# Kernel tuning notes

Hardware: AMD Instinct MI355X
Metric: run time of the kernel (lower is better)

The kernel has to match this reference:

```python
import jax, jax.numpy as jnp
import numpy as np

N, E = 100000, 1600000
IN, ED, H, HL, OUT = 32, 8, 16, 64, 4
BN_EPS = 1e-5


def setup_inputs() -> dict:
    key = jax.random.key(0)
    keys = iter(jax.random.split(key, 64))

    def rn(*s):
        return jax.random.normal(next(keys), s, jnp.float32) * 0.1

    inp = {}
    inp["x"] = jax.random.normal(next(keys), (N, IN), jnp.float32)
    inp["edge_index"] = jax.random.randint(next(keys), (2, E), 0, N)
    inp["edge_attr"] = jax.random.normal(next(keys), (E, ED), jnp.float32)
    for c, din in ((1, IN), (2, H), (3, H)):
        inp[f"ew{c}"] = rn(ED, din)   # GINEConv edge lin: edge_dim -> in_channels
        inp[f"eb{c}"] = rn(din)
        inp[f"wa{c}"] = rn(din, H)    # nn Linear 1
        inp[f"ba{c}"] = rn(H)
        inp[f"g{c}"] = jnp.ones((H,), jnp.float32)    # BN gamma
        inp[f"be{c}"] = jnp.zeros((H,), jnp.float32)  # BN beta
        inp[f"m{c}"] = rn(H)                           # BN running mean
        inp[f"v{c}"] = jax.random.uniform(next(keys), (H,), jnp.float32, 0.5, 1.5)  # BN running var
        inp[f"wb{c}"] = rn(H, H)      # nn Linear 2
        inp[f"bb{c}"] = rn(H)
    inp["lw1"] = rn(3 * H, HL)
    inp["lb1"] = rn(HL)
    inp["lw2"] = rn(HL, OUT)
    inp["lb2"] = rn(OUT)
    return inp


def gine_conv(x, edge_attr, src, dst, ew, eb, wa, ba, g, be, m, v, wb, bb):
    # message: relu(x_j + lin_edge(edge_attr)); aggregate: sum at dst; eps = 0
    e = edge_attr @ ew + eb                      # [E, din]
    msg = jax.nn.relu(x[src] + e)                # [E, din]
    agg = jax.ops.segment_sum(msg, dst, num_segments=x.shape[0])  # [N, din]
    h = (x + agg) @ wa + ba                      # Linear 1
    h = (h - m) * jax.lax.rsqrt(v + BN_EPS) * g + be  # BatchNorm1d (eval)
    h = jax.nn.relu(h)
    h = jax.nn.relu(h @ wb + bb)                 # Linear 2 + ReLU
    return h


def reference(x, edge_index, edge_attr,
              ew1, eb1, wa1, ba1, g1, be1, m1, v1, wb1, bb1,
              ew2, eb2, wa2, ba2, g2, be2, m2, v2, wb2, bb2,
              ew3, eb3, wa3, ba3, g3, be3, m3, v3, wb3, bb3,
              lw1, lb1, lw2, lb2):
    src, dst = edge_index[0], edge_index[1]
    h1 = gine_conv(x, edge_attr, src, dst, ew1, eb1, wa1, ba1, g1, be1, m1, v1, wb1, bb1)
    h2 = gine_conv(h1, edge_attr, src, dst, ew2, eb2, wa2, ba2, g2, be2, m2, v2, wb2, bb2)
    h3 = gine_conv(h2, edge_attr, src, dst, ew3, eb3, wa3, ba3, g3, be3, m3, v3, wb3, bb3)
    h = jnp.concatenate((h1, h2, h3), axis=1)    # [N, 3H]
    h = jax.nn.relu(h @ lw1 + lb1)               # dropout p=0.5 is identity in eval
    return h @ lw2 + lb2                         # [N, OUT]
```

## Files before the change

### kernel.cpp

```cpp
#include <hip/hip_runtime.h>
#include <hip/hip_bf16.h>

#define BN_EPS 1e-5f
#define BINSHIFT 6
#define BINW 64
#define NBLK 256


__global__ __launch_bounds__(256)
void hist2d_kernel(const int* __restrict__ dst, int* __restrict__ histmat,
                   int E, int nbins, int chunk) {
    __shared__ int h[2048];
    for (int i = threadIdx.x; i < nbins; i += 256) h[i] = 0;
    __syncthreads();
    int b = blockIdx.x;
    int e0 = b * chunk;
    int e1 = min(E, e0 + chunk);
    for (int e = e0 + threadIdx.x; e < e1; e += 256)
        atomicAdd(&h[dst[e] >> BINSHIFT], 1);
    __syncthreads();
    int* row = histmat + (size_t)b * nbins;
    for (int i = threadIdx.x; i < nbins; i += 256) row[i] = h[i];
}

__global__ __launch_bounds__(256)
void colsum_kernel(const int* __restrict__ histmat, int* __restrict__ bincnt,
                   int nbins) {
    int bin = blockIdx.x * 256 + threadIdx.x;
    if (bin >= nbins) return;
    int s = 0;
    for (int r = 0; r < NBLK; ++r) s += histmat[(size_t)r * nbins + bin];
    bincnt[bin] = s;
}

__global__ __launch_bounds__(1024)
void bin_scan_kernel(const int* __restrict__ bincnt, int* __restrict__ binstart,
                     int nbins, int E) {
    __shared__ int a[2048];
    __shared__ int b[1024];
    int t = threadIdx.x;
    a[t]        = (t < nbins) ? bincnt[t] : 0;
    a[t + 1024] = (t + 1024 < nbins) ? bincnt[t + 1024] : 0;
    __syncthreads();
    b[t] = a[2 * t] + a[2 * t + 1];
    __syncthreads();
    for (int off = 1; off < 1024; off <<= 1) {
        int v = (t >= off) ? b[t - off] : 0;
        __syncthreads();
        b[t] += v;
        __syncthreads();
    }
    int base = (t == 0) ? 0 : b[t - 1];
    if (2 * t < nbins)     binstart[2 * t]     = base;
    if (2 * t + 1 < nbins) binstart[2 * t + 1] = base + a[2 * t];
    if (t == 0) binstart[nbins] = E;
}

__global__ __launch_bounds__(256)
void rowscan_kernel(int* __restrict__ histmat, const int* __restrict__ binstart,
                    int nbins) {
    __shared__ int a[NBLK];
    int b = blockIdx.x;
    int t = threadIdx.x;
    int v = histmat[(size_t)t * nbins + b];
    a[t] = v;
    __syncthreads();
    for (int off = 1; off < NBLK; off <<= 1) {
        int add = (t >= off) ? a[t - off] : 0;
        __syncthreads();
        a[t] += add;
        __syncthreads();
    }
    histmat[(size_t)t * nbins + b] = binstart[b] + a[t] - v;
}

__global__ __launch_bounds__(256)
void place_kernel(const int* __restrict__ src, const int* __restrict__ dst,
                  const float* __restrict__ edge_attr,
                  const int* __restrict__ histmat,
                  int* __restrict__ tmp_meta, float* __restrict__ tmp_ea,
                  int E, int nbins, int chunk) {
    __shared__ int cur[2048];
    int b = blockIdx.x;
    const int* row = histmat + (size_t)b * nbins;
    for (int i = threadIdx.x; i < nbins; i += 256) cur[i] = row[i];
    __syncthreads();
    int e0 = b * chunk;
    int e1 = min(E, e0 + chunk);
    for (int e = e0 + threadIdx.x; e < e1; e += 256) {
        int d = dst[e];
        int bin = d >> BINSHIFT;
        int pos = atomicAdd(&cur[bin], 1);
        tmp_meta[pos] = ((d & (BINW - 1)) << 20) | src[e];
        const float4* sp = (const float4*)(edge_attr + (size_t)e * 8);
        float4 a0 = sp[0], a1 = sp[1];
        float4* dp = (float4*)(tmp_ea + (size_t)pos * 8);
        dp[0] = a0;
        dp[1] = a1;
    }
}

__global__ __launch_bounds__(256)
void pass2_kernel(const int* __restrict__ binstart, const int* __restrict__ tmp_meta,
                  const float* __restrict__ tmp_ea,
                  int* __restrict__ rowstart, int* __restrict__ src_sorted,
                  float* __restrict__ ea_sorted, int N, int E) {
    __shared__ int s_cur[BINW];
    int b = blockIdx.x;
    int node0 = b << BINSHIFT;
    int e0 = binstart[b], e1 = binstart[b + 1];
    int t = threadIdx.x;

    if (t < BINW) s_cur[t] = 0;
    __syncthreads();

    for (int e = e0 + t; e < e1; e += 256)
        atomicAdd(&s_cur[tmp_meta[e] >> 20], 1);
    __syncthreads();

    if (t < BINW) {
        int val = s_cur[t];
        int inc = val;
#pragma unroll
        for (int off = 1; off < 64; off <<= 1) {
            int n = __shfl_up(inc, off);
            if (t >= off) inc += n;
        }
        int excl = e0 + inc - val;
        s_cur[t] = excl;
        int node = node0 + t;
        if (node <= N) rowstart[node] = excl;
    }
    __syncthreads();

    for (int e = e0 + t; e < e1; e += 256) {
        int mx = tmp_meta[e];
        int dl   = mx >> 20;
        int srcv = mx & 0xFFFFF;
        int fpos = atomicAdd(&s_cur[dl], 1);
        src_sorted[fpos] = srcv;
        const float4* sp = (const float4*)(tmp_ea + (size_t)e * 8);
        float4 a0 = sp[0], a1 = sp[1];
        float4* dp = (float4*)(ea_sorted + (size_t)fpos * 8);
        dp[0] = a0;
        dp[1] = a1;
    }
}

template<int DIN, int C, int S>
__global__ __launch_bounds__(256)
void gine_layer_wave(const float* __restrict__ xin,
                     const int*   __restrict__ rowstart,
                     const int*   __restrict__ src_sorted,
                     const float* __restrict__ ea_sorted,
                     const float* __restrict__ ew, const float* __restrict__ eb,
                     const float* __restrict__ wa, const float* __restrict__ ba,
                     const float* __restrict__ g, const float* __restrict__ be,
                     const float* __restrict__ m, const float* __restrict__ v,
                     const float* __restrict__ wb, const float* __restrict__ bb,
                     float* __restrict__ hout,
                     int N) {
    static_assert(C * S == 64 && C * 4 == DIN, "lane layout");
    constexpr int PAD = DIN + 1;

    __shared__ float s_wa[DIN * 16];
    __shared__ float s_wb[256];
    __shared__ float s_ba[16], s_scale[16], s_shift[16], s_bb[16];
    __shared__ float s_s[16 * PAD];
    __shared__ float s_h[16 * 17];

    int t = threadIdx.x;
    for (int idx = t; idx < DIN * 16; idx += 256) s_wa[idx] = wa[idx];
    s_wb[t] = wb[t];
    if (t < 16) {
        s_ba[t] = ba[t];
        float sc = g[t] * rsqrtf(v[t] + BN_EPS);
        s_scale[t] = sc;
        s_shift[t] = be[t] - m[t] * sc;
        s_bb[t] = bb[t];
    }

    int w    = t >> 6;
    int lane = t & 63;
    int c    = lane / S;
    int s    = lane % S;
    int c0   = c * 4;

    float ew_r[8][4];
#pragma unroll
    for (int k = 0; k < 8; ++k) {
        float4 wv = *(const float4*)(ew + k * DIN + c0);
        ew_r[k][0] = wv.x; ew_r[k][1] = wv.y; ew_r[k][2] = wv.z; ew_r[k][3] = wv.w;
    }
    float4 ebv = *(const float4*)(eb + c0);
    float eb_r[4] = {ebv.x, ebv.y, ebv.z, ebv.w};

    int node0 = blockIdx.x * 16;

#pragma unroll
    for (int q = 0; q < 4; ++q) {
        int nl = w * 4 + q;
        int i  = node0 + nl;
        float acc[4] = {0.f, 0.f, 0.f, 0.f};
        if (i < N) {
            int e0 = rowstart[i];
            int e1 = rowstart[i + 1];
            int e  = e0 + s;
            int sv = (e < e1) ? src_sorted[e] : 0;
            for (; e < e1; e += S) {
                int en = e + S;
                int sv_next = (en < e1) ? src_sorted[en] : 0;
                const float4* ep = (const float4*)(ea_sorted + (size_t)e * 8);
                float4 a0 = ep[0], a1 = ep[1];
                float4 xv = *(const float4*)(xin + (size_t)sv * DIN + c0);
                float av[8] = {a0.x, a0.y, a0.z, a0.w, a1.x, a1.y, a1.z, a1.w};
                float xr[4] = {xv.x, xv.y, xv.z, xv.w};
#pragma unroll
                for (int j = 0; j < 4; ++j) {
                    float lin = eb_r[j];
#pragma unroll
                    for (int k = 0; k < 8; ++k) lin = fmaf(av[k], ew_r[k][j], lin);
                    lin += xr[j];
                    acc[j] += (lin > 0.f ? lin : 0.f);
                }
                sv = sv_next;
            }
        }
#pragma unroll
        for (int mask = S >> 1; mask >= 1; mask >>= 1) {
#pragma unroll
            for (int j = 0; j < 4; ++j) acc[j] += __shfl_xor(acc[j], mask);
        }
        if (s == 0 && i < N) {
            float4 xi = *(const float4*)(xin + (size_t)i * DIN + c0);
            s_s[nl * PAD + c0 + 0] = acc[0] + xi.x;
            s_s[nl * PAD + c0 + 1] = acc[1] + xi.y;
            s_s[nl * PAD + c0 + 2] = acc[2] + xi.z;
            s_s[nl * PAD + c0 + 3] = acc[3] + xi.w;
        }
    }
    __syncthreads();

    int nl2 = t >> 4;
    int j   = t & 15;
    float a = s_ba[j];
#pragma unroll
    for (int k = 0; k < DIN; ++k)
        a = fmaf(s_s[nl2 * PAD + k], s_wa[k * 16 + j], a);
    a = a * s_scale[j] + s_shift[j];
    s_h[nl2 * 17 + j] = a > 0.f ? a : 0.f;
    __syncthreads();

    float o = s_bb[j];
#pragma unroll
    for (int k = 0; k < 16; ++k)
        o = fmaf(s_h[nl2 * 17 + k], s_wb[k * 16 + j], o);
    o = o > 0.f ? o : 0.f;
    int i2 = node0 + nl2;
    if (i2 < N) hout[(size_t)i2 * 16 + j] = o;
}

__global__ __launch_bounds__(256)
void final_kernel(const float* __restrict__ h1, const float* __restrict__ h2,
                  const float* __restrict__ h3,
                  const float* __restrict__ lw1, const float* __restrict__ lb1,
                  const float* __restrict__ lw2, const float* __restrict__ lb2,
                  float* __restrict__ out, int N) {
    constexpr int NPB = 64;
    __shared__ float s_lw1[48 * 64];
    __shared__ float s_lw2[64 * 4];
    __shared__ float s_lb1[64];
    __shared__ float s_lb2[4];
    __shared__ float s_c[NPB][49];

    int t = threadIdx.x;
    for (int idx = t; idx < 48 * 64; idx += 256) s_lw1[idx] = lw1[idx];
    s_lw2[t] = lw2[t];
    if (t < 64) s_lb1[t] = lb1[t];
    if (t < 4) s_lb2[t] = lb2[t];

    int nl = t >> 2;
    int l  = t & 3;
    int i  = blockIdx.x * NPB + nl;

    if (i < N) {
        float4 c1 = ((const float4*)(h1 + (size_t)i * 16))[l];
        float4 c2 = ((const float4*)(h2 + (size_t)i * 16))[l];
        float4 c3 = ((const float4*)(h3 + (size_t)i * 16))[l];
        s_c[nl][l * 4 + 0] = c1.x; s_c[nl][l * 4 + 1] = c1.y;
        s_c[nl][l * 4 + 2] = c1.z; s_c[nl][l * 4 + 3] = c1.w;
        s_c[nl][16 + l * 4 + 0] = c2.x; s_c[nl][16 + l * 4 + 1] = c2.y;
        s_c[nl][16 + l * 4 + 2] = c2.z; s_c[nl][16 + l * 4 + 3] = c2.w;
        s_c[nl][32 + l * 4 + 0] = c3.x; s_c[nl][32 + l * 4 + 1] = c3.y;
        s_c[nl][32 + l * 4 + 2] = c3.z; s_c[nl][32 + l * 4 + 3] = c3.w;
    }
    __syncthreads();

    float o0 = 0.f, o1 = 0.f, o2 = 0.f, o3 = 0.f;
    if (i < N) {
#pragma unroll 4
        for (int jj = 0; jj < 16; ++jj) {
            int j = l * 16 + jj;
            float a = s_lb1[j];
#pragma unroll
            for (int k = 0; k < 48; ++k) a = fmaf(s_c[nl][k], s_lw1[k * 64 + j], a);
            a = a > 0.f ? a : 0.f;
            o0 = fmaf(a, s_lw2[j * 4 + 0], o0);
            o1 = fmaf(a, s_lw2[j * 4 + 1], o1);
            o2 = fmaf(a, s_lw2[j * 4 + 2], o2);
            o3 = fmaf(a, s_lw2[j * 4 + 3], o3);
        }
    }
    o0 += __shfl_xor(o0, 1); o0 += __shfl_xor(o0, 2);
    o1 += __shfl_xor(o1, 1); o1 += __shfl_xor(o1, 2);
    o2 += __shfl_xor(o2, 1); o2 += __shfl_xor(o2, 2);
    o3 += __shfl_xor(o3, 1); o3 += __shfl_xor(o3, 2);
    if (i < N && l == 0) {
        float4 o = {o0 + s_lb2[0], o1 + s_lb2[1], o2 + s_lb2[2], o3 + s_lb2[3]};
        *(float4*)(out + (size_t)i * 4) = o;
    }
}

extern "C" void kernel_launch(void* const* d_in, const int* in_sizes, int n_in,
                              void* d_out, int out_size, void* d_ws, size_t ws_size,
                              hipStream_t stream) {
    const float* x  = (const float*)d_in[0];
    const int*   ei = (const int*)d_in[1];
    const float* ea = (const float*)d_in[2];
    const int N = in_sizes[0] / 32;
    const int E = in_sizes[1] / 2;
    const int* srci = ei;
    const int* dsti = ei + E;

    const float* lw1 = (const float*)d_in[33];
    const float* lb1 = (const float*)d_in[34];
    const float* lw2 = (const float*)d_in[35];
    const float* lb2 = (const float*)d_in[36];

    const int nbins = (N + BINW - 1) >> BINSHIFT;
    const int chunk = (E + NBLK - 1) / NBLK;

    char* p = (char*)d_ws;
    int*   binstart   = (int*)p;   p += (size_t)(nbins + 1 + 3) / 4 * 16;
    int*   bincnt     = (int*)p;   p += (size_t)(nbins + 3) / 4 * 16;
    int*   rowstart   = (int*)p;   p += (size_t)(N + 1 + 3) / 4 * 16;
    int*   histmat    = (int*)p;   p += (size_t)NBLK * nbins * 4;
    int*   src_sorted = (int*)p;   p += (size_t)E * 4;
    float* ea_sorted  = (float*)p; p += (size_t)E * 8 * 4;
    char*  u          = p;
    int*   tmp_meta   = (int*)u;
    float* tmp_ea     = (float*)(u + (size_t)E * 4);
    float* h1         = (float*)u;
    float* h2         = h1 + (size_t)N * 16;
    float* h3         = h2 + (size_t)N * 16;

    hist2d_kernel<<<NBLK, 256, 0, stream>>>(dsti, histmat, E, nbins, chunk);
    colsum_kernel<<<(nbins + 255) / 256, 256, 0, stream>>>(histmat, bincnt, nbins);
    bin_scan_kernel<<<1, 1024, 0, stream>>>(bincnt, binstart, nbins, E);
    rowscan_kernel<<<nbins, NBLK, 0, stream>>>(histmat, binstart, nbins);
    place_kernel<<<NBLK, 256, 0, stream>>>(srci, dsti, ea, histmat,
                                           tmp_meta, tmp_ea, E, nbins, chunk);
    pass2_kernel<<<nbins, 256, 0, stream>>>(binstart, tmp_meta, tmp_ea,
                                            rowstart, src_sorted, ea_sorted,
                                            N, E);

    const int lblocks = (N + 15) / 16;
    gine_layer_wave<32, 8, 8><<<lblocks, 256, 0, stream>>>(
        x, rowstart, src_sorted, ea_sorted,
        (const float*)d_in[3], (const float*)d_in[4],
        (const float*)d_in[5], (const float*)d_in[6],
        (const float*)d_in[7], (const float*)d_in[8],
        (const float*)d_in[9], (const float*)d_in[10],
        (const float*)d_in[11], (const float*)d_in[12], h1, N);

    gine_layer_wave<16, 4, 16><<<lblocks, 256, 0, stream>>>(
        h1, rowstart, src_sorted, ea_sorted,
        (const float*)d_in[13], (const float*)d_in[14],
        (const float*)d_in[15], (const float*)d_in[16],
        (const float*)d_in[17], (const float*)d_in[18],
        (const float*)d_in[19], (const float*)d_in[20],
        (const float*)d_in[21], (const float*)d_in[22], h2, N);

    gine_layer_wave<16, 4, 16><<<lblocks, 256, 0, stream>>>(
        h2, rowstart, src_sorted, ea_sorted,
        (const float*)d_in[23], (const float*)d_in[24],
        (const float*)d_in[25], (const float*)d_in[26],
        (const float*)d_in[27], (const float*)d_in[28],
        (const float*)d_in[29], (const float*)d_in[30],
        (const float*)d_in[31], (const float*)d_in[32], h3, N);

    final_kernel<<<(N + 63) / 64, 256, 0, stream>>>(
        h1, h2, h3, lw1, lb1, lw2, lb2, (float*)d_out, N);
}
```

Measured before the change: 526.8 us.

## Pack sorted edge attributes as bf16 and raise binning block count

Edge attributes are rounded to bf16 and packed into one 16-byte record when placed into bins, so the two sort passes and the three layer kernels each move half the edge-attribute bytes. The counting-sort block count goes from 256 to 1024, and chunks are assigned to blocks through an interleaving map. The column-sum loop gets unroll 8 and rowscan's launch bound is raised to match. This trades precision on the edge features, which may change results beyond tolerance, for lower memory traffic. It also makes the histogram matrix and the per-bin scans larger.

```diff
diff --git a/kernel.cpp b/kernel.cpp
--- a/kernel.cpp
+++ b/kernel.cpp
@@ -4,7 +4,21 @@
 #define BN_EPS 1e-5f
 #define BINSHIFT 6
 #define BINW 64
-#define NBLK 256
+#define NBLK 1024
+
+__device__ __forceinline__ unsigned pk_bf16(float x, float y) {
+    unsigned ux = __float_as_uint(x);
+    ux += 0x7FFFu + ((ux >> 16) & 1u);
+    unsigned uy = __float_as_uint(y);
+    uy += 0x7FFFu + ((uy >> 16) & 1u);
+    return (ux >> 16) | (uy & 0xFFFF0000u);
+}
+__device__ __forceinline__ float bf_lo(unsigned u) { return __uint_as_float(u << 16); }
+__device__ __forceinline__ float bf_hi(unsigned u) { return __uint_as_float(u & 0xFFFF0000u); }
+
+__device__ __forceinline__ int chunk_of(int bid) {
+    return ((bid & 7) << 7) | (bid >> 3);
+}
 
 
 __global__ __launch_bounds__(256)
@@ -13,13 +27,13 @@
     __shared__ int h[2048];
     for (int i = threadIdx.x; i < nbins; i += 256) h[i] = 0;
     __syncthreads();
-    int b = blockIdx.x;
-    int e0 = b * chunk;
+    int c = chunk_of(blockIdx.x);
+    int e0 = c * chunk;
     int e1 = min(E, e0 + chunk);
     for (int e = e0 + threadIdx.x; e < e1; e += 256)
         atomicAdd(&h[dst[e] >> BINSHIFT], 1);
     __syncthreads();
-    int* row = histmat + (size_t)b * nbins;
+    int* row = histmat + (size_t)c * nbins;
     for (int i = threadIdx.x; i < nbins; i += 256) row[i] = h[i];
 }
 
@@ -29,6 +43,7 @@
     int bin = blockIdx.x * 256 + threadIdx.x;
     if (bin >= nbins) return;
     int s = 0;
+#pragma unroll 8
     for (int r = 0; r < NBLK; ++r) s += histmat[(size_t)r * nbins + bin];
     bincnt[bin] = s;
 }
@@ -56,7 +71,7 @@
     if (t == 0) binstart[nbins] = E;
 }
 
-__global__ __launch_bounds__(256)
+__global__ __launch_bounds__(1024)
 void rowscan_kernel(int* __restrict__ histmat, const int* __restrict__ binstart,
                     int nbins) {
     __shared__ int a[NBLK];
@@ -78,14 +93,14 @@
 void place_kernel(const int* __restrict__ src, const int* __restrict__ dst,
                   const float* __restrict__ edge_attr,
                   const int* __restrict__ histmat,
-                  int* __restrict__ tmp_meta, float* __restrict__ tmp_ea,
+                  int* __restrict__ tmp_meta, uint4* __restrict__ tmp_ea,
                   int E, int nbins, int chunk) {
     __shared__ int cur[2048];
-    int b = blockIdx.x;
-    const int* row = histmat + (size_t)b * nbins;
+    int c = chunk_of(blockIdx.x);
+    const int* row = histmat + (size_t)c * nbins;
     for (int i = threadIdx.x; i < nbins; i += 256) cur[i] = row[i];
     __syncthreads();
-    int e0 = b * chunk;
+    int e0 = c * chunk;
     int e1 = min(E, e0 + chunk);
     for (int e = e0 + threadIdx.x; e < e1; e += 256) {
         int d = dst[e];
@@ -94,17 +109,20 @@
         tmp_meta[pos] = ((d & (BINW - 1)) << 20) | src[e];
         const float4* sp = (const float4*)(edge_attr + (size_t)e * 8);
         float4 a0 = sp[0], a1 = sp[1];
-        float4* dp = (float4*)(tmp_ea + (size_t)pos * 8);
-        dp[0] = a0;
-        dp[1] = a1;
+        uint4 pkd;
+        pkd.x = pk_bf16(a0.x, a0.y);
+        pkd.y = pk_bf16(a0.z, a0.w);
+        pkd.z = pk_bf16(a1.x, a1.y);
+        pkd.w = pk_bf16(a1.z, a1.w);
+        tmp_ea[pos] = pkd;
     }
 }
 
 __global__ __launch_bounds__(256)
 void pass2_kernel(const int* __restrict__ binstart, const int* __restrict__ tmp_meta,
-                  const float* __restrict__ tmp_ea,
+                  const uint4* __restrict__ tmp_ea,
                   int* __restrict__ rowstart, int* __restrict__ src_sorted,
-                  float* __restrict__ ea_sorted, int N, int E) {
+                  uint4* __restrict__ ea_sorted, int N, int E) {
     __shared__ int s_cur[BINW];
     int b = blockIdx.x;
     int node0 = b << BINSHIFT;
@@ -139,11 +157,7 @@
         int srcv = mx & 0xFFFFF;
         int fpos = atomicAdd(&s_cur[dl], 1);
         src_sorted[fpos] = srcv;
-        const float4* sp = (const float4*)(tmp_ea + (size_t)e * 8);
-        float4 a0 = sp[0], a1 = sp[1];
-        float4* dp = (float4*)(ea_sorted + (size_t)fpos * 8);
-        dp[0] = a0;
-        dp[1] = a1;
+        ea_sorted[fpos] = tmp_ea[e];
     }
 }
 
@@ -152,7 +166,7 @@
 void gine_layer_wave(const float* __restrict__ xin,
                      const int*   __restrict__ rowstart,
                      const int*   __restrict__ src_sorted,
-                     const float* __restrict__ ea_sorted,
+                     const uint4* __restrict__ ea_sorted,
                      const float* __restrict__ ew, const float* __restrict__ eb,
                      const float* __restrict__ wa, const float* __restrict__ ba,
                      const float* __restrict__ g, const float* __restrict__ be,
@@ -210,10 +224,10 @@
             for (; e < e1; e += S) {
                 int en = e + S;
                 int sv_next = (en < e1) ? src_sorted[en] : 0;
-                const float4* ep = (const float4*)(ea_sorted + (size_t)e * 8);
-                float4 a0 = ep[0], a1 = ep[1];
+                uint4 ev = ea_sorted[e];
                 float4 xv = *(const float4*)(xin + (size_t)sv * DIN + c0);
-                float av[8] = {a0.x, a0.y, a0.z, a0.w, a1.x, a1.y, a1.z, a1.w};
+                float av[8] = {bf_lo(ev.x), bf_hi(ev.x), bf_lo(ev.y), bf_hi(ev.y),
+                               bf_lo(ev.z), bf_hi(ev.z), bf_lo(ev.w), bf_hi(ev.w)};
                 float xr[4] = {xv.x, xv.y, xv.z, xv.w};
 #pragma unroll
                 for (int j = 0; j < 4; ++j) {
@@ -346,10 +360,10 @@
     int*   rowstart   = (int*)p;   p += (size_t)(N + 1 + 3) / 4 * 16;
     int*   histmat    = (int*)p;   p += (size_t)NBLK * nbins * 4;
     int*   src_sorted = (int*)p;   p += (size_t)E * 4;
-    float* ea_sorted  = (float*)p; p += (size_t)E * 8 * 4;
+    uint4* ea_sorted  = (uint4*)p; p += (size_t)E * 16;
     char*  u          = p;
     int*   tmp_meta   = (int*)u;
-    float* tmp_ea     = (float*)(u + (size_t)E * 4);
+    uint4* tmp_ea     = (uint4*)(u + (size_t)E * 4);
     float* h1         = (float*)u;
     float* h2         = h1 + (size_t)N * 16;
     float* h3         = h2 + (size_t)N * 16;
```

Result: no change. 519.4 us (-1.4%).
